# Performance work log

Measured on AMD Instinct MI355X. Metric: run time of the kernel, lower is better.

The kernel has to match this reference:

```python
import jax, jax.numpy as jnp
import numpy as np

D = 384      # n_embed_dims
H = 6        # n_heads
HS = D // H  # head_size = 64
T = 256      # block_size
B = 256
EPS = 1e-5


def setup_inputs() -> dict:
    key = jax.random.key(0)
    ks = jax.random.split(key, 12)
    s_in = 1.0 / np.sqrt(D)
    s_ff = 1.0 / np.sqrt(4 * D)
    return {
        "x": jax.random.normal(ks[0], (B, T, D), jnp.float32),
        # per-head QKV weights, stacked [H, D, HS] (Linear bias=False)
        "wq": jax.random.normal(ks[1], (H, D, HS), jnp.float32) * s_in,
        "wk": jax.random.normal(ks[2], (H, D, HS), jnp.float32) * s_in,
        "wv": jax.random.normal(ks[3], (H, D, HS), jnp.float32) * s_in,
        "w_proj": jax.random.normal(ks[4], (D, D), jnp.float32) * s_in,
        "b_proj": jax.random.normal(ks[5], (D,), jnp.float32) * s_in,
        "w1": jax.random.normal(ks[6], (D, 4 * D), jnp.float32) * s_in,
        "b1": jax.random.normal(ks[7], (4 * D,), jnp.float32) * s_in,
        "w2": jax.random.normal(ks[8], (4 * D, D), jnp.float32) * s_ff,
        "b2": jax.random.normal(ks[9], (D,), jnp.float32) * s_ff,
        "g1": jnp.ones((D,), jnp.float32),
        "be1": jnp.zeros((D,), jnp.float32),
        "g2": jnp.ones((D,), jnp.float32),
        "be2": jnp.zeros((D,), jnp.float32),
    }


def _layernorm(x, g, b):
    mu = jnp.mean(x, axis=-1, keepdims=True)
    var = jnp.mean(jnp.square(x - mu), axis=-1, keepdims=True)
    return (x - mu) * jax.lax.rsqrt(var + EPS) * g + b


def _attention(x, wq, wk, wv, w_proj, b_proj):
    # faithful quirk: scale = 1/sqrt(C) with C = full embed dim (384)
    scale = 1.0 / jnp.sqrt(jnp.asarray(D, x.dtype))
    q = jnp.einsum("btd,hde->bhte", x, wq)  # [B,H,T,HS]
    k = jnp.einsum("btd,hde->bhte", x, wk)
    v = jnp.einsum("btd,hde->bhte", x, wv)
    w = jnp.einsum("bhte,bhse->bhts", q, k) * scale  # [B,H,T,T], no mask
    w = jax.nn.softmax(w, axis=-1)
    out = jnp.einsum("bhts,bhse->bhte", w, v)  # [B,H,T,HS]
    # concat heads along feature dim (head order matches torch cat)
    out = out.transpose(0, 2, 1, 3).reshape(x.shape[0], x.shape[1], D)
    return out @ w_proj + b_proj


def reference(x, wq, wk, wv, w_proj, b_proj, w1, b1, w2, b2, g1, be1, g2, be2):
    x = x + _attention(_layernorm(x, g1, be1), wq, wk, wv, w_proj, b_proj)
    h = _layernorm(x, g2, be2)
    h = jax.nn.relu(h @ w1 + b1) @ w2 + b2  # dropout = eval-mode identity
    return x + h
```

## Files before the change

### kernel.cpp

```cpp
#include <hip/hip_runtime.h>
#include <stdint.h>

#define NTOK 65536
#define DE 384
#define QSTR 1280

typedef __bf16 bf16x8 __attribute__((ext_vector_type(8)));
typedef float  f32x4 __attribute__((ext_vector_type(4)));
typedef unsigned short u16x8 __attribute__((ext_vector_type(8)));

__device__ __forceinline__ unsigned short f2bf(float f) {
  union { float fl; unsigned u; } a; a.fl = f;
  unsigned r = a.u + 0x7fffu + ((a.u >> 16) & 1u);
  return (unsigned short)(r >> 16);
}

__device__ __forceinline__ void gll16(const void* g, void* l) {
  __builtin_amdgcn_global_load_lds((const __attribute__((address_space(1))) void*)g,
                                   (__attribute__((address_space(3))) void*)l, 16, 0, 0);
}

__device__ __forceinline__ bf16x8 ds128(unsigned addr) {
  bf16x8 r;
  asm volatile("ds_read_b128 %0, %1" : "=v"(r) : "v"(addr));
  return r;
}

__global__ void pack_t(unsigned short* __restrict__ dst, const float* __restrict__ src,
                       int R, int C) {
  int t = blockIdx.x * 256 + threadIdx.x;
  if (t >= R * C) return;
  int r = t / C, c = t - r * C;
  dst[(size_t)c * R + r] = f2bf(src[t]);
}

__global__ void qkv_pack(const float* __restrict__ wq, const float* __restrict__ wk,
                         const float* __restrict__ wv, unsigned short* __restrict__ dst) {
  int t = blockIdx.x * 256 + threadIdx.x;
  if (t >= QSTR * 384) return;
  int n = t / 384, k = t - n * 384;
  unsigned short v = 0;
  if (n < 1152) {
    int which = n / 384, r = n - which * 384;
    const float* src = which == 0 ? wq : (which == 1 ? wk : wv);
    int h = r >> 6, e = r & 63;
    v = f2bf(src[h * 24576 + k * 64 + e]);
  }
  dst[t] = v;
}

__global__ __launch_bounds__(256) void ln_kernel(const float* __restrict__ x,
                                                 const float* __restrict__ g,
                                                 const float* __restrict__ be,
                                                 unsigned short* __restrict__ out) {
  int wave = threadIdx.x >> 6, lane = threadIdx.x & 63;
  size_t row = (size_t)blockIdx.x * 4 + wave;
  const float* xr = x + row * DE;
  int c0 = lane * 2;
  float2 v0 = *(const float2*)(xr + c0);
  float2 v1 = *(const float2*)(xr + 128 + c0);
  float2 v2 = *(const float2*)(xr + 256 + c0);
  float s  = v0.x + v0.y + v1.x + v1.y + v2.x + v2.y;
  float ss = v0.x*v0.x + v0.y*v0.y + v1.x*v1.x + v1.y*v1.y + v2.x*v2.x + v2.y*v2.y;
#pragma unroll
  for (int m = 1; m < 64; m <<= 1) { s += __shfl_xor(s, m); ss += __shfl_xor(ss, m); }
  float mu = s * (1.0f / 384.0f);
  float rstd = rsqrtf(ss * (1.0f / 384.0f) - mu * mu + 1e-5f);
  unsigned short* orow = out + row * DE;
  {
    float a0 = (v0.x - mu) * rstd * g[c0] + be[c0];
    float a1 = (v0.y - mu) * rstd * g[c0 + 1] + be[c0 + 1];
    *(unsigned*)(orow + c0) = (unsigned)f2bf(a0) | ((unsigned)f2bf(a1) << 16);
  }
  {
    int c = c0 + 128;
    float a0 = (v1.x - mu) * rstd * g[c] + be[c];
    float a1 = (v1.y - mu) * rstd * g[c + 1] + be[c + 1];
    *(unsigned*)(orow + c) = (unsigned)f2bf(a0) | ((unsigned)f2bf(a1) << 16);
  }
  {
    int c = c0 + 256;
    float a0 = (v2.x - mu) * rstd * g[c] + be[c];
    float a1 = (v2.y - mu) * rstd * g[c + 1] + be[c + 1];
    *(unsigned*)(orow + c) = (unsigned)f2bf(a0) | ((unsigned)f2bf(a1) << 16);
  }
}

template<int EPI, int BM, int BN, int WM, int WN>
__device__ __forceinline__
void gemm_core(const unsigned short* __restrict__ A, const unsigned short* __restrict__ Bt,
               int M, int N, int K, int ntx,
               const float* __restrict__ bias, const float* __restrict__ resid,
               float* __restrict__ outf, unsigned short* __restrict__ outb) {
  constexpr int T = WM * WN * 64;
  constexpr int MWT = BM / WM, NWT = BN / WN;
  constexpr int MF = MWT / 16, NF = NWT / 16;
  constexpr int MH = MF / 4;
  constexpr int LA = (BM * 128) / (T * 16);
  constexpr int LB = (BN * 128) / (T * 16);
  __shared__ __align__(16) unsigned short As[2][BM * 64];
  __shared__ __align__(16) unsigned short Bs[2][BN * 64];
  const int tid = threadIdx.x;
  const int wave = tid >> 6, lane = tid & 63;

  const int nwg = gridDim.x;
  const int cpx = nwg >> 3;
  const int wg = (blockIdx.x & 7) * cpx + (blockIdx.x >> 3);
  const int bx = wg % ntx, by = wg / ntx;
  const int mBase = by * BM, nBase = bx * BN;
  const int wmi = wave / WN, wni = wave % WN;
  const int wm = wmi * MWT, wn = wni * NWT;
  const int fr = lane & 15, fg = lane >> 4;

  const unsigned asb = (unsigned)(uintptr_t)&As[0][0];
  const unsigned bsb = (unsigned)(uintptr_t)&Bs[0][0];

  f32x4 acc[MF][NF];
  const f32x4 z = {0.f, 0.f, 0.f, 0.f};
#pragma unroll
  for (int i = 0; i < MF; ++i)
#pragma unroll
    for (int j = 0; j < NF; ++j) acc[i][j] = z;

  auto stage = [&](int buf, int kt) {
#pragma unroll
    for (int i = 0; i < LA; ++i) {
      int Lb = i * (T * 16) + wave * 1024;
      int L = Lb + lane * 16;
      int row = L >> 7;
      int col = (((L >> 4) & 7) ^ (row & 7)) << 3;
      gll16(A + (size_t)(mBase + row) * K + kt + col, (unsigned short*)As[buf] + (Lb >> 1));
    }
#pragma unroll
    for (int i = 0; i < LB; ++i) {
      int Lb = i * (T * 16) + wave * 1024;
      int L = Lb + lane * 16;
      int row = L >> 7;
      int col = (((L >> 4) & 7) ^ (row & 7)) << 3;
      gll16(Bt + (size_t)(nBase + row) * K + kt + col, (unsigned short*)Bs[buf] + (Lb >> 1));
    }
  };

  const int NK = K >> 6;
  stage(0, 0);
  for (int t = 0; t < NK; ++t) {
    const int cur = t & 1;
    if (t + 1 < NK) {
      stage(cur ^ 1, (t + 1) << 6);
      if constexpr (LA + LB == 8) asm volatile("s_waitcnt vmcnt(8)" ::: "memory");
      else                        asm volatile("s_waitcnt vmcnt(6)" ::: "memory");
    } else {
      asm volatile("s_waitcnt vmcnt(0)" ::: "memory");
    }
    asm volatile("" ::: "memory");
    __builtin_amdgcn_s_barrier();
    asm volatile("" ::: "memory");

    const unsigned ab = asb + (cur ? (unsigned)(BM * 128) : 0u);
    const unsigned bb = bsb + (cur ? (unsigned)(BN * 128) : 0u);
#pragma unroll
    for (int ks = 0; ks < 2; ++ks) {
      bf16x8 bfr[NF];
#pragma unroll
      for (int nb = 0; nb < NF; ++nb) {
        int row = wn + nb * 16 + fr;
        unsigned byte = (unsigned)(row << 7) + ((unsigned)((ks * 4 + fg) ^ (row & 7)) << 4);
        bfr[nb] = ds128(bb + byte);
      }
#pragma unroll
      for (int mh = 0; mh < MH; ++mh) {
        bf16x8 af[4];
#pragma unroll
        for (int mb = 0; mb < 4; ++mb) {
          int row = wm + (mh * 4 + mb) * 16 + fr;
          unsigned byte = (unsigned)(row << 7) + ((unsigned)((ks * 4 + fg) ^ (row & 7)) << 4);
          af[mb] = ds128(ab + byte);
        }
        asm volatile("s_waitcnt lgkmcnt(0)" ::: "memory");
        __builtin_amdgcn_sched_barrier(0);
        __builtin_amdgcn_s_setprio(1);
#pragma unroll
        for (int mb = 0; mb < 4; ++mb)
#pragma unroll
          for (int nb = 0; nb < NF; ++nb)
            acc[mh * 4 + mb][nb] =
                __builtin_amdgcn_mfma_f32_16x16x32_bf16(af[mb], bfr[nb], acc[mh * 4 + mb][nb], 0, 0, 0);
        __builtin_amdgcn_s_setprio(0);
      }
    }
    asm volatile("" ::: "memory");
    __builtin_amdgcn_s_barrier();
    asm volatile("" ::: "memory");
  }

#pragma unroll
  for (int mb = 0; mb < MF; ++mb) {
#pragma unroll
    for (int nb = 0; nb < NF; ++nb) {
      const int gn = nBase + wn + nb * 16 + fr;
#pragma unroll
      for (int i = 0; i < 4; ++i) {
        const int gm = mBase + wm + mb * 16 + (fg << 2) + i;
        float val = acc[mb][nb][i];
        if (EPI == 0) {
          outb[(size_t)gm * N + gn] = f2bf(val);
        } else if (EPI == 1) {
          size_t idx = (size_t)gm * N + gn;
          outf[idx] = val + bias[gn] + resid[idx];
        } else if (EPI == 2) {
          float r = val + bias[gn];
          outb[(size_t)gm * N + gn] = f2bf(r > 0.f ? r : 0.f);
        } else {
          size_t idx = (size_t)gm * N + gn;
          outf[idx] = val + bias[gn] + resid[idx];
        }
      }
    }
  }
}

__global__ __launch_bounds__(512, 1)
void gemm_qkv(const unsigned short* __restrict__ A, const unsigned short* __restrict__ Bt,
              int M, int N, int K, int ntx, const float* __restrict__ bias,
              const float* __restrict__ resid, float* __restrict__ outf,
              unsigned short* __restrict__ outb) {
  gemm_core<0, 256, 256, 2, 4>(A, Bt, M, N, K, ntx, bias, resid, outf, outb);
}
__global__ __launch_bounds__(512, 1)
void gemm_proj(const unsigned short* __restrict__ A, const unsigned short* __restrict__ Bt,
               int M, int N, int K, int ntx, const float* __restrict__ bias,
               const float* __restrict__ resid, float* __restrict__ outf,
               unsigned short* __restrict__ outb) {
  gemm_core<1, 256, 128, 4, 2>(A, Bt, M, N, K, ntx, bias, resid, outf, outb);
}
__global__ __launch_bounds__(512, 1)
void gemm_mlp1(const unsigned short* __restrict__ A, const unsigned short* __restrict__ Bt,
               int M, int N, int K, int ntx, const float* __restrict__ bias,
               const float* __restrict__ resid, float* __restrict__ outf,
               unsigned short* __restrict__ outb) {
  gemm_core<2, 256, 256, 2, 4>(A, Bt, M, N, K, ntx, bias, resid, outf, outb);
}
__global__ __launch_bounds__(512, 1)
void gemm_mlp2(const unsigned short* __restrict__ A, const unsigned short* __restrict__ Bt,
               int M, int N, int K, int ntx, const float* __restrict__ bias,
               const float* __restrict__ resid, float* __restrict__ outf,
               unsigned short* __restrict__ outb) {
  gemm_core<3, 256, 128, 4, 2>(A, Bt, M, N, K, ntx, bias, resid, outf, outb);
}

__global__ __launch_bounds__(256)
void attn_kernel(const unsigned short* __restrict__ qkvn, unsigned short* __restrict__ o) {
  __shared__ unsigned short Vt[64 * 256];
  __shared__ unsigned short Pw[4][64 * 32];
  const int bh = blockIdx.x;
  const int b = bh / 6, h = bh - b * 6;
  const unsigned short* base = qkvn + (size_t)(b * 256) * QSTR;
  const unsigned short* qb = base + h * 64;
  const unsigned short* kbp = base + 384 + h * 64;
  const unsigned short* vbp = base + 768 + h * 64;
  const int wave = threadIdx.x >> 6, lane = threadIdx.x & 63;
  const int fr = lane & 15, fg = lane >> 4;
  const int fk = fg << 3;
  const int qrow0 = wave << 6;
  const float scale = 0.051031036307982884f;
  const f32x4 z = {0.f, 0.f, 0.f, 0.f};

  {
    const int s = threadIdx.x;
    u16x8 v8[8];
#pragma unroll
    for (int j = 0; j < 8; ++j)
      v8[j] = *(const u16x8*)(vbp + (size_t)s * QSTR + j * 8);
#pragma unroll
    for (int e = 0; e < 64; ++e)
      Vt[(e << 8) + (s ^ ((e & 7) << 3))] = v8[e >> 3][e & 7];
  }
  __syncthreads();

  bf16x8 qf[4][2];
#pragma unroll
  for (int rb = 0; rb < 4; ++rb)
#pragma unroll
    for (int ks = 0; ks < 2; ++ks)
      qf[rb][ks] = *(const bf16x8*)(qb + (size_t)(qrow0 + rb * 16 + fr) * QSTR + ks * 32 + fk);

  float pm[4][4];
#pragma unroll
  for (int rb = 0; rb < 4; ++rb)
#pragma unroll
    for (int i = 0; i < 4; ++i) pm[rb][i] = -1e30f;

  for (int cb = 0; cb < 16; ++cb) {
    bf16x8 kf0 = *(const bf16x8*)(kbp + (size_t)(cb * 16 + fr) * QSTR + fk);
    bf16x8 kf1 = *(const bf16x8*)(kbp + (size_t)(cb * 16 + fr) * QSTR + 32 + fk);
#pragma unroll
    for (int rb = 0; rb < 4; ++rb) {
      f32x4 s = __builtin_amdgcn_mfma_f32_16x16x32_bf16(qf[rb][0], kf0, z, 0, 0, 0);
      s = __builtin_amdgcn_mfma_f32_16x16x32_bf16(qf[rb][1], kf1, s, 0, 0, 0);
#pragma unroll
      for (int i = 0; i < 4; ++i) pm[rb][i] = fmaxf(pm[rb][i], s[i]);
    }
  }
#pragma unroll
  for (int rb = 0; rb < 4; ++rb)
#pragma unroll
    for (int i = 0; i < 4; ++i) {
      float v = pm[rb][i];
      v = fmaxf(v, __shfl_xor(v, 1));
      v = fmaxf(v, __shfl_xor(v, 2));
      v = fmaxf(v, __shfl_xor(v, 4));
      v = fmaxf(v, __shfl_xor(v, 8));
      pm[rb][i] = v;
    }

  f32x4 oacc[4][4];
  float psum[4][4];
#pragma unroll
  for (int rb = 0; rb < 4; ++rb)
#pragma unroll
    for (int nb = 0; nb < 4; ++nb) oacc[rb][nb] = z;
#pragma unroll
  for (int rb = 0; rb < 4; ++rb)
#pragma unroll
    for (int i = 0; i < 4; ++i) psum[rb][i] = 0.f;

  for (int kb2 = 0; kb2 < 8; ++kb2) {
#pragma unroll
    for (int c2 = 0; c2 < 2; ++c2) {
      int cb = kb2 * 2 + c2;
      bf16x8 kf0 = *(const bf16x8*)(kbp + (size_t)(cb * 16 + fr) * QSTR + fk);
      bf16x8 kf1 = *(const bf16x8*)(kbp + (size_t)(cb * 16 + fr) * QSTR + 32 + fk);
#pragma unroll
      for (int rb = 0; rb < 4; ++rb) {
        f32x4 s = __builtin_amdgcn_mfma_f32_16x16x32_bf16(qf[rb][0], kf0, z, 0, 0, 0);
        s = __builtin_amdgcn_mfma_f32_16x16x32_bf16(qf[rb][1], kf1, s, 0, 0, 0);
#pragma unroll
        for (int i = 0; i < 4; ++i) {
          float p = __expf(scale * (s[i] - pm[rb][i]));
          psum[rb][i] += p;
          Pw[wave][(rb * 16 + (fg << 2) + i) * 32 + c2 * 16 + fr] = f2bf(p);
        }
      }
    }
    bf16x8 pa[4], vf[4];
#pragma unroll
    for (int rb = 0; rb < 4; ++rb) pa[rb] = *(const bf16x8*)(&Pw[wave][(rb * 16 + fr) * 32 + fk]);
#pragma unroll
    for (int nb = 0; nb < 4; ++nb) {
      int e = nb * 16 + fr;
      vf[nb] = *(const bf16x8*)(&Vt[(e << 8) + ((kb2 * 32 + fk) ^ ((e & 7) << 3))]);
    }
#pragma unroll
    for (int rb = 0; rb < 4; ++rb)
#pragma unroll
      for (int nb = 0; nb < 4; ++nb)
        oacc[rb][nb] = __builtin_amdgcn_mfma_f32_16x16x32_bf16(pa[rb], vf[nb], oacc[rb][nb], 0, 0, 0);
  }

  float rs[4][4];
#pragma unroll
  for (int rb = 0; rb < 4; ++rb)
#pragma unroll
    for (int i = 0; i < 4; ++i) {
      float v = psum[rb][i];
      v += __shfl_xor(v, 1);
      v += __shfl_xor(v, 2);
      v += __shfl_xor(v, 4);
      v += __shfl_xor(v, 8);
      rs[rb][i] = 1.0f / v;
    }

#pragma unroll
  for (int rb = 0; rb < 4; ++rb)
#pragma unroll
    for (int nb = 0; nb < 4; ++nb)
#pragma unroll
      for (int i = 0; i < 4; ++i) {
        int token = b * 256 + qrow0 + rb * 16 + (fg << 2) + i;
        int gcol = h * 64 + nb * 16 + fr;
        o[(size_t)token * DE + gcol] = f2bf(oacc[rb][nb][i] * rs[rb][i]);
      }
}

extern "C" void kernel_launch(void* const* d_in, const int* in_sizes, int n_in,
                              void* d_out, int out_size, void* d_ws, size_t ws_size,
                              hipStream_t stream) {
  const float* x     = (const float*)d_in[0];
  const float* wq    = (const float*)d_in[1];
  const float* wk    = (const float*)d_in[2];
  const float* wv    = (const float*)d_in[3];
  const float* wproj = (const float*)d_in[4];
  const float* bproj = (const float*)d_in[5];
  const float* w1    = (const float*)d_in[6];
  const float* b1    = (const float*)d_in[7];
  const float* w2    = (const float*)d_in[8];
  const float* b2    = (const float*)d_in[9];
  const float* g1    = (const float*)d_in[10];
  const float* be1   = (const float*)d_in[11];
  const float* g2    = (const float*)d_in[12];
  const float* be2   = (const float*)d_in[13];

  char* ws = (char*)d_ws;
  unsigned short* xln   = (unsigned short*)(ws + 0);
  float*          x1    = (float*)(ws + 0);
  unsigned short* qkvn  = (unsigned short*)(ws + 50331648);
  unsigned short* hbuf  = (unsigned short*)(ws + 100663296);
  unsigned short* act   = (unsigned short*)(ws + 150994944);
  unsigned short* attno = (unsigned short*)(ws + 218103808);
  unsigned short* wqkvt = (unsigned short*)(ws + 352321536);
  unsigned short* wprjt = (unsigned short*)(ws + 352321536 + 983040);
  unsigned short* w1t   = (unsigned short*)(ws + 352321536 + 983040 + 294912);
  unsigned short* w2t   = (unsigned short*)(ws + 352321536 + 983040 + 294912 + 1179648);

  qkv_pack<<<(QSTR * 384 + 255) / 256, 256, 0, stream>>>(wq, wk, wv, wqkvt);
  pack_t<<<(147456 + 255) / 256, 256, 0, stream>>>(wprjt, wproj, 384, 384);
  pack_t<<<(589824 + 255) / 256, 256, 0, stream>>>(w1t, w1, 384, 1536);
  pack_t<<<(589824 + 255) / 256, 256, 0, stream>>>(w2t, w2, 1536, 384);

  ln_kernel<<<NTOK / 4, 256, 0, stream>>>(x, g1, be1, xln);

  gemm_qkv<<<5 * 256, 512, 0, stream>>>(xln, wqkvt, NTOK, QSTR, 384, 5,
                                        nullptr, nullptr, nullptr, qkvn);

  attn_kernel<<<1536, 256, 0, stream>>>(qkvn, attno);

  gemm_proj<<<3 * 256, 512, 0, stream>>>(attno, wprjt, NTOK, 384, 384, 3,
                                         bproj, x, x1, nullptr);

  ln_kernel<<<NTOK / 4, 256, 0, stream>>>(x1, g2, be2, hbuf);

  gemm_mlp1<<<6 * 256, 512, 0, stream>>>(hbuf, w1t, NTOK, 1536, 384, 6,
                                         b1, nullptr, nullptr, act);

  gemm_mlp2<<<3 * 256, 512, 0, stream>>>(act, w2t, NTOK, 384, 1536, 3,
                                         b2, x1, (float*)d_out, nullptr);
}
```

Measured before the change: 559.1 us.

## Restructure GEMM mainloop into 4-stage K=32 pipeline with interleaved prefetch

The GEMM core moves from a double-buffered K=64 tile to a four-buffer ring of K=32 tiles with prefetch distance two. Global-to-LDS loads are split and interleaved between the two MFMA halves, and one barrier per iteration replaces two. The LDS layout changes to pair rows into 128-byte swizzled lines to suit the narrower K tile. The aim is to hide load latency better and cut barrier stalls, at the cost of more loop iterations and more complex address math. With prefetch distance two on a four-buffer ring, a buffer being read may not be overwritten, so a single barrier could be enough.

```diff
diff --git a/kernel.cpp b/kernel.cpp
--- a/kernel.cpp
+++ b/kernel.cpp
@@ -24,6 +24,15 @@
   bf16x8 r;
   asm volatile("ds_read_b128 %0, %1" : "=v"(r) : "v"(addr));
   return r;
+}
+
+template<int N> __device__ __forceinline__ void wait_vmcnt() {
+  if constexpr (N == 0) asm volatile("s_waitcnt vmcnt(0)" ::: "memory");
+  else if constexpr (N == 3) asm volatile("s_waitcnt vmcnt(3)" ::: "memory");
+  else if constexpr (N == 4) asm volatile("s_waitcnt vmcnt(4)" ::: "memory");
+  else if constexpr (N == 5) asm volatile("s_waitcnt vmcnt(5)" ::: "memory");
+  else if constexpr (N == 6) asm volatile("s_waitcnt vmcnt(6)" ::: "memory");
+  else asm volatile("s_waitcnt vmcnt(8)" ::: "memory");
 }
 
 __global__ void pack_t(unsigned short* __restrict__ dst, const float* __restrict__ src,
@@ -92,14 +101,14 @@
                int M, int N, int K, int ntx,
                const float* __restrict__ bias, const float* __restrict__ resid,
                float* __restrict__ outf, unsigned short* __restrict__ outb) {
-  constexpr int T = WM * WN * 64;
   constexpr int MWT = BM / WM, NWT = BN / WN;
   constexpr int MF = MWT / 16, NF = NWT / 16;
-  constexpr int MH = MF / 4;
-  constexpr int LA = (BM * 128) / (T * 16);
-  constexpr int LB = (BN * 128) / (T * 16);
-  __shared__ __align__(16) unsigned short As[2][BM * 64];
-  __shared__ __align__(16) unsigned short Bs[2][BN * 64];
+  constexpr int MHF = MF / 2;
+  constexpr int LA = (BM * 64) / 8192;
+  constexpr int LB = (BN * 64) / 8192;
+  constexpr int LT = LA + LB;
+  __shared__ __align__(16) unsigned short As[4][BM * 32];
+  __shared__ __align__(16) unsigned short Bs[4][BN * 32];
   const int tid = threadIdx.x;
   const int wave = tid >> 6, lane = tid & 63;
 
@@ -108,8 +117,7 @@
   const int wg = (blockIdx.x & 7) * cpx + (blockIdx.x >> 3);
   const int bx = wg % ntx, by = wg / ntx;
   const int mBase = by * BM, nBase = bx * BN;
-  const int wmi = wave / WN, wni = wave % WN;
-  const int wm = wmi * MWT, wn = wni * NWT;
+  const int wm = (wave / WN) * MWT, wn = (wave % WN) * NWT;
   const int fr = lane & 15, fg = lane >> 4;
 
   const unsigned asb = (unsigned)(uintptr_t)&As[0][0];
@@ -122,75 +130,84 @@
 #pragma unroll
     for (int j = 0; j < NF; ++j) acc[i][j] = z;
 
-  auto stage = [&](int buf, int kt) {
-#pragma unroll
-    for (int i = 0; i < LA; ++i) {
-      int Lb = i * (T * 16) + wave * 1024;
+  auto stage_one = [&](int buf, int kt, int idx) {
+    if (idx < LA) {
+      int Lb = idx * 8192 + wave * 1024;
       int L = Lb + lane * 16;
-      int row = L >> 7;
-      int col = (((L >> 4) & 7) ^ (row & 7)) << 3;
-      gll16(A + (size_t)(mBase + row) * K + kt + col, (unsigned short*)As[buf] + (Lb >> 1));
-    }
-#pragma unroll
-    for (int i = 0; i < LB; ++i) {
-      int Lb = i * (T * 16) + wave * 1024;
+      int p = L >> 7;
+      int sl = ((L >> 4) & 7) ^ (p & 7);
+      int m = (p << 1) | (sl >> 2);
+      int col = (sl & 3) << 3;
+      gll16(A + (size_t)(mBase + m) * K + kt + col, (unsigned short*)As[buf] + (Lb >> 1));
+    } else {
+      int Lb = (idx - LA) * 8192 + wave * 1024;
       int L = Lb + lane * 16;
-      int row = L >> 7;
-      int col = (((L >> 4) & 7) ^ (row & 7)) << 3;
-      gll16(Bt + (size_t)(nBase + row) * K + kt + col, (unsigned short*)Bs[buf] + (Lb >> 1));
+      int p = L >> 7;
+      int sl = ((L >> 4) & 7) ^ (p & 7);
+      int m = (p << 1) | (sl >> 2);
+      int col = (sl & 3) << 3;
+      gll16(Bt + (size_t)(nBase + m) * K + kt + col, (unsigned short*)Bs[buf] + (Lb >> 1));
     }
   };
 
-  const int NK = K >> 6;
-  stage(0, 0);
+  auto fraddr = [&](unsigned base, int row) -> unsigned {
+    return base + ((unsigned)(row >> 1) << 7) +
+           ((unsigned)((fg | ((row & 1) << 2)) ^ ((row >> 1) & 7)) << 4);
+  };
+
+  const int NK = K >> 5;
+#pragma unroll
+  for (int i = 0; i < LT; ++i) stage_one(0, 0, i);
+#pragma unroll
+  for (int i = 0; i < LT; ++i) stage_one(1, 32, i);
+
   for (int t = 0; t < NK; ++t) {
-    const int cur = t & 1;
-    if (t + 1 < NK) {
-      stage(cur ^ 1, (t + 1) << 6);
-      if constexpr (LA + LB == 8) asm volatile("s_waitcnt vmcnt(8)" ::: "memory");
-      else                        asm volatile("s_waitcnt vmcnt(6)" ::: "memory");
-    } else {
-      asm volatile("s_waitcnt vmcnt(0)" ::: "memory");
-    }
-    asm volatile("" ::: "memory");
+    const int cb = t & 3;
+    if (t + 1 < NK) wait_vmcnt<LT>();
+    else            wait_vmcnt<0>();
     __builtin_amdgcn_s_barrier();
-    asm volatile("" ::: "memory");
-
-    const unsigned ab = asb + (cur ? (unsigned)(BM * 128) : 0u);
-    const unsigned bb = bsb + (cur ? (unsigned)(BN * 128) : 0u);
-#pragma unroll
-    for (int ks = 0; ks < 2; ++ks) {
-      bf16x8 bfr[NF];
-#pragma unroll
-      for (int nb = 0; nb < NF; ++nb) {
-        int row = wn + nb * 16 + fr;
-        unsigned byte = (unsigned)(row << 7) + ((unsigned)((ks * 4 + fg) ^ (row & 7)) << 4);
-        bfr[nb] = ds128(bb + byte);
-      }
-#pragma unroll
-      for (int mh = 0; mh < MH; ++mh) {
-        bf16x8 af[4];
-#pragma unroll
-        for (int mb = 0; mb < 4; ++mb) {
-          int row = wm + (mh * 4 + mb) * 16 + fr;
-          unsigned byte = (unsigned)(row << 7) + ((unsigned)((ks * 4 + fg) ^ (row & 7)) << 4);
-          af[mb] = ds128(ab + byte);
-        }
-        asm volatile("s_waitcnt lgkmcnt(0)" ::: "memory");
-        __builtin_amdgcn_sched_barrier(0);
-        __builtin_amdgcn_s_setprio(1);
-#pragma unroll
-        for (int mb = 0; mb < 4; ++mb)
-#pragma unroll
-          for (int nb = 0; nb < NF; ++nb)
-            acc[mh * 4 + mb][nb] =
-                __builtin_amdgcn_mfma_f32_16x16x32_bf16(af[mb], bfr[nb], acc[mh * 4 + mb][nb], 0, 0, 0);
-        __builtin_amdgcn_s_setprio(0);
-      }
-    }
-    asm volatile("" ::: "memory");
-    __builtin_amdgcn_s_barrier();
-    asm volatile("" ::: "memory");
+
+    const unsigned ab = asb + (unsigned)cb * (BM * 64);
+    const unsigned bb = bsb + (unsigned)cb * (BN * 64);
+    const bool pf = (t + 2) < NK;
+    const int pbuf = (t + 2) & 3;
+    const int pkt = (t + 2) << 5;
+
+    bf16x8 bfr[NF];
+    bf16x8 af[MHF];
+#pragma unroll
+    for (int nb = 0; nb < NF; ++nb) bfr[nb] = ds128(fraddr(bb, wn + nb * 16 + fr));
+#pragma unroll
+    for (int mb = 0; mb < MHF; ++mb) af[mb] = ds128(fraddr(ab, wm + mb * 16 + fr));
+    if (pf) {
+      stage_one(pbuf, pkt, 0);
+      if (LT > 1) stage_one(pbuf, pkt, 1);
+    }
+    asm volatile("s_waitcnt lgkmcnt(0)" ::: "memory");
+    __builtin_amdgcn_sched_barrier(0);
+    __builtin_amdgcn_s_setprio(1);
+#pragma unroll
+    for (int mb = 0; mb < MHF; ++mb)
+#pragma unroll
+      for (int nb = 0; nb < NF; ++nb)
+        acc[mb][nb] = __builtin_amdgcn_mfma_f32_16x16x32_bf16(af[mb], bfr[nb], acc[mb][nb], 0, 0, 0);
+    __builtin_amdgcn_s_setprio(0);
+#pragma unroll
+    for (int mb = 0; mb < MHF; ++mb) af[mb] = ds128(fraddr(ab, wm + (MHF + mb) * 16 + fr));
+    if (pf) {
+#pragma unroll
+      for (int i = 2; i < LT; ++i) stage_one(pbuf, pkt, i);
+    }
+    asm volatile("s_waitcnt lgkmcnt(0)" ::: "memory");
+    __builtin_amdgcn_sched_barrier(0);
+    __builtin_amdgcn_s_setprio(1);
+#pragma unroll
+    for (int mb = 0; mb < MHF; ++mb)
+#pragma unroll
+      for (int nb = 0; nb < NF; ++nb)
+        acc[MHF + mb][nb] =
+            __builtin_amdgcn_mfma_f32_16x16x32_bf16(af[mb], bfr[nb], acc[MHF + mb][nb], 0, 0, 0);
+    __builtin_amdgcn_s_setprio(0);
   }
 
 #pragma unroll
```

New measurement: 571.1 us. +2.2%, slower.

## Switch GEMMs to 128x128 tiles with BK=32 and four workgroups per CU

Applied to the files above, without the earlier changes.

All four GEMMs move from large 256x256/256x128 tiles with 512 threads and one workgroup per CU to fixed 128x128 tiles, 256 threads, a K-step of 32, and launch bounds allowing four workgroups per CU. The LDS layout changes to pack two 32-element rows per 128-byte line with a new XOR swizzle. The aim is more occupancy and better latency hiding across workgroups, and finer grids that balance better over the CUs. The cost is less data reuse per tile, twice as many barriers per K, and more global traffic per FLOP.

```diff
diff --git a/kernel.cpp b/kernel.cpp
--- a/kernel.cpp
+++ b/kernel.cpp
@@ -86,20 +86,14 @@
   }
 }
 
-template<int EPI, int BM, int BN, int WM, int WN>
+template<int EPI>
 __device__ __forceinline__
 void gemm_core(const unsigned short* __restrict__ A, const unsigned short* __restrict__ Bt,
                int M, int N, int K, int ntx,
                const float* __restrict__ bias, const float* __restrict__ resid,
                float* __restrict__ outf, unsigned short* __restrict__ outb) {
-  constexpr int T = WM * WN * 64;
-  constexpr int MWT = BM / WM, NWT = BN / WN;
-  constexpr int MF = MWT / 16, NF = NWT / 16;
-  constexpr int MH = MF / 4;
-  constexpr int LA = (BM * 128) / (T * 16);
-  constexpr int LB = (BN * 128) / (T * 16);
-  __shared__ __align__(16) unsigned short As[2][BM * 64];
-  __shared__ __align__(16) unsigned short Bs[2][BN * 64];
+  __shared__ __align__(16) unsigned short As[2][4096];
+  __shared__ __align__(16) unsigned short Bs[2][4096];
   const int tid = threadIdx.x;
   const int wave = tid >> 6, lane = tid & 63;
 
@@ -107,48 +101,46 @@
   const int cpx = nwg >> 3;
   const int wg = (blockIdx.x & 7) * cpx + (blockIdx.x >> 3);
   const int bx = wg % ntx, by = wg / ntx;
-  const int mBase = by * BM, nBase = bx * BN;
-  const int wmi = wave / WN, wni = wave % WN;
-  const int wm = wmi * MWT, wn = wni * NWT;
+  const int mBase = by << 7, nBase = bx << 7;
+  const int wm = (wave >> 1) << 6, wn = (wave & 1) << 6;
   const int fr = lane & 15, fg = lane >> 4;
 
   const unsigned asb = (unsigned)(uintptr_t)&As[0][0];
   const unsigned bsb = (unsigned)(uintptr_t)&Bs[0][0];
 
-  f32x4 acc[MF][NF];
+  f32x4 acc[4][4];
   const f32x4 z = {0.f, 0.f, 0.f, 0.f};
 #pragma unroll
-  for (int i = 0; i < MF; ++i)
-#pragma unroll
-    for (int j = 0; j < NF; ++j) acc[i][j] = z;
+  for (int i = 0; i < 4; ++i)
+#pragma unroll
+    for (int j = 0; j < 4; ++j) acc[i][j] = z;
 
   auto stage = [&](int buf, int kt) {
 #pragma unroll
-    for (int i = 0; i < LA; ++i) {
-      int Lb = i * (T * 16) + wave * 1024;
+    for (int i = 0; i < 2; ++i) {
+      int Lb = i * 4096 + wave * 1024;
       int L = Lb + lane * 16;
-      int row = L >> 7;
-      int col = (((L >> 4) & 7) ^ (row & 7)) << 3;
-      gll16(A + (size_t)(mBase + row) * K + kt + col, (unsigned short*)As[buf] + (Lb >> 1));
-    }
-#pragma unroll
-    for (int i = 0; i < LB; ++i) {
-      int Lb = i * (T * 16) + wave * 1024;
-      int L = Lb + lane * 16;
-      int row = L >> 7;
-      int col = (((L >> 4) & 7) ^ (row & 7)) << 3;
-      gll16(Bt + (size_t)(nBase + row) * K + kt + col, (unsigned short*)Bs[buf] + (Lb >> 1));
+      int p = L >> 7;
+      int sl = ((L >> 4) & 7) ^ (p & 7);
+      int m = (p << 1) | (sl >> 2);
+      int col = (sl & 3) << 3;
+      gll16(A + (size_t)(mBase + m) * K + kt + col, (unsigned short*)As[buf] + (Lb >> 1));
+      gll16(Bt + (size_t)(nBase + m) * K + kt + col, (unsigned short*)Bs[buf] + (Lb >> 1));
     }
   };
 
-  const int NK = K >> 6;
+  auto fraddr = [&](unsigned base, int row) -> unsigned {
+    return base + ((unsigned)(row >> 1) << 7) +
+           ((unsigned)((fg | ((row & 1) << 2)) ^ ((row >> 1) & 7)) << 4);
+  };
+
+  const int NK = K >> 5;
   stage(0, 0);
   for (int t = 0; t < NK; ++t) {
     const int cur = t & 1;
     if (t + 1 < NK) {
-      stage(cur ^ 1, (t + 1) << 6);
-      if constexpr (LA + LB == 8) asm volatile("s_waitcnt vmcnt(8)" ::: "memory");
-      else                        asm volatile("s_waitcnt vmcnt(6)" ::: "memory");
+      stage(cur ^ 1, (t + 1) << 5);
+      asm volatile("s_waitcnt vmcnt(4)" ::: "memory");
     } else {
       asm volatile("s_waitcnt vmcnt(0)" ::: "memory");
     }
@@ -156,47 +148,31 @@
     __builtin_amdgcn_s_barrier();
     asm volatile("" ::: "memory");
 
-    const unsigned ab = asb + (cur ? (unsigned)(BM * 128) : 0u);
-    const unsigned bb = bsb + (cur ? (unsigned)(BN * 128) : 0u);
-#pragma unroll
-    for (int ks = 0; ks < 2; ++ks) {
-      bf16x8 bfr[NF];
-#pragma unroll
-      for (int nb = 0; nb < NF; ++nb) {
-        int row = wn + nb * 16 + fr;
-        unsigned byte = (unsigned)(row << 7) + ((unsigned)((ks * 4 + fg) ^ (row & 7)) << 4);
-        bfr[nb] = ds128(bb + byte);
-      }
-#pragma unroll
-      for (int mh = 0; mh < MH; ++mh) {
-        bf16x8 af[4];
-#pragma unroll
-        for (int mb = 0; mb < 4; ++mb) {
-          int row = wm + (mh * 4 + mb) * 16 + fr;
-          unsigned byte = (unsigned)(row << 7) + ((unsigned)((ks * 4 + fg) ^ (row & 7)) << 4);
-          af[mb] = ds128(ab + byte);
-        }
-        asm volatile("s_waitcnt lgkmcnt(0)" ::: "memory");
-        __builtin_amdgcn_sched_barrier(0);
-        __builtin_amdgcn_s_setprio(1);
-#pragma unroll
-        for (int mb = 0; mb < 4; ++mb)
-#pragma unroll
-          for (int nb = 0; nb < NF; ++nb)
-            acc[mh * 4 + mb][nb] =
-                __builtin_amdgcn_mfma_f32_16x16x32_bf16(af[mb], bfr[nb], acc[mh * 4 + mb][nb], 0, 0, 0);
-        __builtin_amdgcn_s_setprio(0);
-      }
-    }
+    const unsigned ab = asb + (cur ? 8192u : 0u);
+    const unsigned bb = bsb + (cur ? 8192u : 0u);
+    bf16x8 af[4], bfr[4];
+#pragma unroll
+    for (int nb = 0; nb < 4; ++nb) bfr[nb] = ds128(fraddr(bb, wn + nb * 16 + fr));
+#pragma unroll
+    for (int mb = 0; mb < 4; ++mb) af[mb] = ds128(fraddr(ab, wm + mb * 16 + fr));
+    asm volatile("s_waitcnt lgkmcnt(0)" ::: "memory");
+    __builtin_amdgcn_sched_barrier(0);
+    __builtin_amdgcn_s_setprio(1);
+#pragma unroll
+    for (int mb = 0; mb < 4; ++mb)
+#pragma unroll
+      for (int nb = 0; nb < 4; ++nb)
+        acc[mb][nb] = __builtin_amdgcn_mfma_f32_16x16x32_bf16(af[mb], bfr[nb], acc[mb][nb], 0, 0, 0);
+    __builtin_amdgcn_s_setprio(0);
     asm volatile("" ::: "memory");
     __builtin_amdgcn_s_barrier();
     asm volatile("" ::: "memory");
   }
 
 #pragma unroll
-  for (int mb = 0; mb < MF; ++mb) {
-#pragma unroll
-    for (int nb = 0; nb < NF; ++nb) {
+  for (int mb = 0; mb < 4; ++mb) {
+#pragma unroll
+    for (int nb = 0; nb < 4; ++nb) {
       const int gn = nBase + wn + nb * 16 + fr;
 #pragma unroll
       for (int i = 0; i < 4; ++i) {
@@ -219,33 +195,33 @@
   }
 }
 
-__global__ __launch_bounds__(512, 1)
+__global__ __launch_bounds__(256, 4)
 void gemm_qkv(const unsigned short* __restrict__ A, const unsigned short* __restrict__ Bt,
               int M, int N, int K, int ntx, const float* __restrict__ bias,
               const float* __restrict__ resid, float* __restrict__ outf,
               unsigned short* __restrict__ outb) {
-  gemm_core<0, 256, 256, 2, 4>(A, Bt, M, N, K, ntx, bias, resid, outf, outb);
-}
-__global__ __launch_bounds__(512, 1)
+  gemm_core<0>(A, Bt, M, N, K, ntx, bias, resid, outf, outb);
+}
+__global__ __launch_bounds__(256, 4)
 void gemm_proj(const unsigned short* __restrict__ A, const unsigned short* __restrict__ Bt,
                int M, int N, int K, int ntx, const float* __restrict__ bias,
                const float* __restrict__ resid, float* __restrict__ outf,
                unsigned short* __restrict__ outb) {
-  gemm_core<1, 256, 128, 4, 2>(A, Bt, M, N, K, ntx, bias, resid, outf, outb);
-}
-__global__ __launch_bounds__(512, 1)
+  gemm_core<1>(A, Bt, M, N, K, ntx, bias, resid, outf, outb);
+}
+__global__ __launch_bounds__(256, 4)
 void gemm_mlp1(const unsigned short* __restrict__ A, const unsigned short* __restrict__ Bt,
                int M, int N, int K, int ntx, const float* __restrict__ bias,
                const float* __restrict__ resid, float* __restrict__ outf,
                unsigned short* __restrict__ outb) {
-  gemm_core<2, 256, 256, 2, 4>(A, Bt, M, N, K, ntx, bias, resid, outf, outb);
-}
-__global__ __launch_bounds__(512, 1)
+  gemm_core<2>(A, Bt, M, N, K, ntx, bias, resid, outf, outb);
+}
+__global__ __launch_bounds__(256, 4)
 void gemm_mlp2(const unsigned short* __restrict__ A, const unsigned short* __restrict__ Bt,
                int M, int N, int K, int ntx, const float* __restrict__ bias,
                const float* __restrict__ resid, float* __restrict__ outf,
                unsigned short* __restrict__ outb) {
-  gemm_core<3, 256, 128, 4, 2>(A, Bt, M, N, K, ntx, bias, resid, outf, outb);
+  gemm_core<3>(A, Bt, M, N, K, ntx, bias, resid, outf, outb);
 }
 
 __global__ __launch_bounds__(256)
@@ -419,19 +395,19 @@
 
   ln_kernel<<<NTOK / 4, 256, 0, stream>>>(x, g1, be1, xln);
 
-  gemm_qkv<<<5 * 256, 512, 0, stream>>>(xln, wqkvt, NTOK, QSTR, 384, 5,
-                                        nullptr, nullptr, nullptr, qkvn);
+  gemm_qkv<<<10 * 512, 256, 0, stream>>>(xln, wqkvt, NTOK, QSTR, 384, 10,
+                                         nullptr, nullptr, nullptr, qkvn);
 
   attn_kernel<<<1536, 256, 0, stream>>>(qkvn, attno);
 
-  gemm_proj<<<3 * 256, 512, 0, stream>>>(attno, wprjt, NTOK, 384, 384, 3,
+  gemm_proj<<<3 * 512, 256, 0, stream>>>(attno, wprjt, NTOK, 384, 384, 3,
                                          bproj, x, x1, nullptr);
 
   ln_kernel<<<NTOK / 4, 256, 0, stream>>>(x1, g2, be2, hbuf);
 
-  gemm_mlp1<<<6 * 256, 512, 0, stream>>>(hbuf, w1t, NTOK, 1536, 384, 6,
-                                         b1, nullptr, nullptr, act);
-
-  gemm_mlp2<<<3 * 256, 512, 0, stream>>>(act, w2t, NTOK, 384, 1536, 3,
+  gemm_mlp1<<<12 * 512, 256, 0, stream>>>(hbuf, w1t, NTOK, 1536, 384, 12,
+                                          b1, nullptr, nullptr, act);
+
+  gemm_mlp2<<<3 * 512, 256, 0, stream>>>(act, w2t, NTOK, 384, 1536, 3,
                                          b2, x1, (float*)d_out, nullptr);
 }
```

New measurement: 575.3 us. 1.03x slower.
